# Optimization experiments

Hardware: AMD Instinct MI355X
Metric: run time of the kernel (lower is better)

The kernel has to match this reference:

```python
import jax, jax.numpy as jnp
import numpy as np

IN_FEATURES = 4096
OUT_FEATURES = 16384

def setup_inputs() -> dict:
    key = jax.random.key(0)
    k1, k2 = jax.random.split(key)
    x = jax.random.normal(k1, (4, 2048, IN_FEATURES), dtype=jnp.float32)
    # init_weights: uniform(-1, 1)
    W = jax.random.uniform(k2, (OUT_FEATURES, IN_FEATURES), dtype=jnp.float32, minval=-1.0, maxval=1.0)
    b = jnp.zeros((OUT_FEATURES,), dtype=jnp.float32)
    return {"x": x, "W": W, "b": b}

def reference(x, W, b):
    # Binarize weights to {-1, 0, +1} via sign, then dense linear: y = x @ sign(W)^T + b
    Wb = jnp.sign(W)
    return jnp.einsum('bsd,od->bso', x, Wb) + b
```

## Files before the change

### kernel.cpp

```cpp
#include <hip/hip_runtime.h>
#include <hip/hip_bf16.h>

#define M_TOT 8192
#define N_TOT 16384
#define K_TOT 4096
#define BM 256
#define BN 128
#define BK 64
#define NT (K_TOT / BK)

typedef int i32x4 __attribute__((ext_vector_type(4)));
typedef int i32x16 __attribute__((ext_vector_type(16)));
typedef __bf16 bf16x8 __attribute__((ext_vector_type(8)));
typedef float f32x4 __attribute__((ext_vector_type(4)));

#define GLOAD_LDS16(g, l)                                                     \
  __builtin_amdgcn_global_load_lds(                                           \
      (__attribute__((address_space(1))) const void*)(g),                     \
      (__attribute__((address_space(3))) void*)(l), 16, 0, 0)

__device__ __forceinline__ ushort f2bf_rne(float f) {
  unsigned u = __float_as_uint(f);
  u += 0x7FFFu + ((u >> 16) & 1u);
  return (ushort)(u >> 16);
}
__device__ __forceinline__ ushort sgn_bf16(float w) {
  return w > 0.f ? (ushort)0x3F80u : (w < 0.f ? (ushort)0xBF80u : (ushort)0u);
}


__global__ void quant_x_kernel(const float* __restrict__ x,
                               char* __restrict__ At, float* __restrict__ s) {
  int row = blockIdx.x;
  int tid = threadIdx.x;
  const float4* xr = (const float4*)(x + (size_t)row * K_TOT + tid * 16);
  float4 v[4];
  float amax = 0.f;
#pragma unroll
  for (int j = 0; j < 4; ++j) {
    v[j] = xr[j];
    amax = fmaxf(amax, fmaxf(fmaxf(fabsf(v[j].x), fabsf(v[j].y)),
                             fmaxf(fabsf(v[j].z), fabsf(v[j].w))));
  }
#pragma unroll
  for (int o = 32; o > 0; o >>= 1) amax = fmaxf(amax, __shfl_xor(amax, o));
  __shared__ float wmax[4];
  if ((tid & 63) == 0) wmax[tid >> 6] = amax;
  __syncthreads();
  amax = fmaxf(fmaxf(wmax[0], wmax[1]), fmaxf(wmax[2], wmax[3]));
  float inv = amax > 0.f ? 127.0f / amax : 0.f;
  if (tid == 0) s[row] = amax * (1.0f / 127.0f);
  int q[16];
#pragma unroll
  for (int j = 0; j < 4; ++j) {
    q[j * 4 + 0] = max(-127, min(127, __float2int_rn(v[j].x * inv)));
    q[j * 4 + 1] = max(-127, min(127, __float2int_rn(v[j].y * inv)));
    q[j * 4 + 2] = max(-127, min(127, __float2int_rn(v[j].z * inv)));
    q[j * 4 + 3] = max(-127, min(127, __float2int_rn(v[j].w * inv)));
  }
  int4 o4;
  int* op = (int*)&o4;
#pragma unroll
  for (int j = 0; j < 4; ++j)
    op[j] = (q[j * 4] & 255) | ((q[j * 4 + 1] & 255) << 8) |
            ((q[j * 4 + 2] & 255) << 16) | ((q[j * 4 + 3] & 255) << 24);
  int r32 = row >> 5, l31 = row & 31;
  int kt = tid >> 2, ks = (tid >> 1) & 1, hi = tid & 1;
  size_t dst = ((size_t)(r32 * 128 + kt * 2 + ks) << 10) + ((hi * 32 + l31) << 4);
  *(int4*)(At + dst) = o4;
}

__global__ void quant_w_kernel(const float* __restrict__ w,
                               char* __restrict__ Bt) {
  int n32 = blockIdx.x;
  int t = threadIdx.x;
#pragma unroll 4
  for (int i = 0; i < 32; ++i) {
    int c = i * 256 + t;
    int kt = c >> 7, ks = (c >> 6) & 1, l = c & 63;
    int n = n32 * 32 + (l & 31);
    int k = kt * 64 + ks * 32 + (l >> 5) * 16;
    const float4* src = (const float4*)(w + (size_t)n * K_TOT + k);
    int4 o4;
    int* op = (int*)&o4;
#pragma unroll
    for (int j = 0; j < 4; ++j) {
      float4 v = src[j];
      int q0 = v.x > 0.f ? 1 : (v.x < 0.f ? -1 : 0);
      int q1 = v.y > 0.f ? 1 : (v.y < 0.f ? -1 : 0);
      int q2 = v.z > 0.f ? 1 : (v.z < 0.f ? -1 : 0);
      int q3 = v.w > 0.f ? 1 : (v.w < 0.f ? -1 : 0);
      op[j] = (q0 & 255) | ((q1 & 255) << 8) | ((q2 & 255) << 16) |
              ((q3 & 255) << 24);
    }
    *(int4*)(Bt + ((size_t)n32 << 17) + ((size_t)c << 4)) = o4;
  }
}

__global__ __launch_bounds__(256, 2) void gemm_i8_reg(
    const char* __restrict__ At, const char* __restrict__ Bt,
    const float* __restrict__ s, const float* __restrict__ bias,
    float* __restrict__ C) {
  __shared__ char lds[4][16384];

  int bid = blockIdx.x;
  int wg = (bid & 7) * 512 + (bid >> 3);
  int bnS = wg >> 9;
  int rem = wg & 511;
  int bm = rem >> 4;
  int bn = bnS * 16 + (rem & 15);
  int rowBase = bm * BM;
  int colBase = bn * BN;

  int t = threadIdx.x;
  int lane = t & 63;
  int wave = t >> 6;
  int wr = wave >> 1;
  int wc = wave & 1;
  int l31 = lane & 31;
  int hi = lane >> 5;

  const char* gAp[4];
#pragma unroll
  for (int q = 0; q < 4; ++q) {
    int ss = t + 256 * q;
    int g = ss >> 6;
    int ks = g >> 3, rg = g & 7;
    gAp[q] = At + ((size_t)((bm * 8 + rg) * 128 + ks) << 10) + ((ss & 63) << 4);
  }
  const char* gBp[2];
#pragma unroll
  for (int ni = 0; ni < 2; ++ni)
    gBp[ni] = Bt + ((size_t)(bn * 4 + wc * 2 + ni) << 17) + (lane << 4);

  i32x16 acc[4][2] = {};
  i32x4 brA[2][2], brB[2][2];

#define STAGE_A(kt_, buf_)                                                    \
  {                                                                           \
    size_t _o = (size_t)(kt_) << 11;                                          \
    GLOAD_LDS16(gAp[0] + _o, &lds[buf_][t * 16]);                             \
    GLOAD_LDS16(gAp[1] + _o, &lds[buf_][4096 + t * 16]);                      \
    GLOAD_LDS16(gAp[2] + _o, &lds[buf_][8192 + t * 16]);                      \
    GLOAD_LDS16(gAp[3] + _o, &lds[buf_][12288 + t * 16]);                     \
  }
#define LOADB(kt_, dst)                                                       \
  {                                                                           \
    size_t _o = (size_t)(kt_) << 11;                                          \
    dst[0][0] = *(const i32x4*)(gBp[0] + _o);                                 \
    dst[0][1] = *(const i32x4*)(gBp[1] + _o);                                 \
    dst[1][0] = *(const i32x4*)(gBp[0] + _o + 1024);                          \
    dst[1][1] = *(const i32x4*)(gBp[1] + _o + 1024);                          \
  }
#define COMPUTE(buf_, bset)                                                   \
  {                                                                           \
    const char* _la = &lds[buf_][0];                                          \
    _Pragma("unroll") for (int ks = 0; ks < 2; ++ks) {                        \
      _Pragma("unroll") for (int mi = 0; mi < 4; ++mi) {                      \
        i32x4 _af = *(const i32x4*)(_la + ((ks * 8 + wr * 4 + mi) << 10) +    \
                                    (lane << 4));                             \
        acc[mi][0] = __builtin_amdgcn_mfma_i32_32x32x32_i8(                   \
            _af, bset[ks][0], acc[mi][0], 0, 0, 0);                           \
        acc[mi][1] = __builtin_amdgcn_mfma_i32_32x32x32_i8(                   \
            _af, bset[ks][1], acc[mi][1], 0, 0, 0);                           \
      }                                                                       \
    }                                                                         \
  }
#define TILE(kt_, buf_, bcur, bnxt, VMC)                                      \
  {                                                                           \
    STAGE_A((kt_) + 2, ((buf_) + 2) & 3);                                     \
    LOADB((kt_) + 1, bnxt);                                                   \
    asm volatile("s_waitcnt vmcnt(" #VMC ")" ::: "memory");                   \
    COMPUTE(buf_, bcur);                                                      \
    __builtin_amdgcn_s_barrier();                                             \
  }

  STAGE_A(0, 0);
  STAGE_A(1, 1);
  LOADB(0, brA);
  asm volatile("s_waitcnt vmcnt(0)" ::: "memory");
  __builtin_amdgcn_s_barrier();

  for (int it = 0; it < 15; ++it) {
    int kt = it * 4;
    TILE(kt + 0, 0, brA, brB, 8);
    TILE(kt + 1, 1, brB, brA, 8);
    TILE(kt + 2, 2, brA, brB, 8);
    TILE(kt + 3, 3, brB, brA, 8);
  }
  {
    STAGE_A(62, 2);
    LOADB(61, brB);
    asm volatile("s_waitcnt vmcnt(8)" ::: "memory");
    COMPUTE(0, brA);
    __builtin_amdgcn_s_barrier();

    STAGE_A(63, 3);
    LOADB(62, brA);
    asm volatile("s_waitcnt vmcnt(8)" ::: "memory");
    COMPUTE(1, brB);
    __builtin_amdgcn_s_barrier();

    LOADB(63, brB);
    asm volatile("s_waitcnt vmcnt(4)" ::: "memory");
    COMPUTE(2, brA);
    __builtin_amdgcn_s_barrier();

    asm volatile("s_waitcnt vmcnt(0)" ::: "memory");
    COMPUTE(3, brB);
  }

#undef TILE
#undef COMPUTE
#undef LOADB
#undef STAGE_A

#pragma unroll
  for (int mi = 0; mi < 4; ++mi) {
#pragma unroll
    for (int ni = 0; ni < 2; ++ni) {
      int gc = colBase + wc * 64 + ni * 32 + l31;
      float bv = bias[gc];
#pragma unroll
      for (int rg = 0; rg < 16; ++rg) {
        int rowIn = (rg & 3) + 8 * (rg >> 2) + 4 * hi;
        int gr = rowBase + wr * 128 + mi * 32 + rowIn;
        C[(size_t)gr * N_TOT + gc] = (float)acc[mi][ni][rg] * s[gr] + bv;
      }
    }
  }
}

__global__ void gemm_fused_kernel(const float* __restrict__ A,
                                  const float* __restrict__ W,
                                  const float* __restrict__ bias,
                                  float* __restrict__ C) {
  __shared__ ushort lsA[128 * 32];
  __shared__ ushort lsB[128 * 32];

  int nwg = gridDim.x;
  int bid = blockIdx.x;
  int wg = (bid & 7) * (nwg >> 3) + (bid >> 3);
  const int NBN = N_TOT / 128;
  int bm = wg / NBN;
  int bn = wg % NBN;
  int rowBase = bm * 128;
  int colBase = bn * 128;

  int t = threadIdx.x;
  int lane = t & 63;
  int wave = t >> 6;
  int wm = (wave >> 1) * 64;
  int wn = (wave & 1) * 64;

  f32x4 acc[4][4] = {};

  int srow = t >> 3;
  int scol = (t & 7) * 4;
  int fr = lane & 15;
  int koff = (lane >> 4) * 8;

  for (int k0 = 0; k0 < K_TOT; k0 += 32) {
    float4 va[4], vb[4];
#pragma unroll
    for (int r = 0; r < 4; ++r) {
      va[r] = *(const float4*)&A[(size_t)(rowBase + r * 32 + srow) * K_TOT + k0 + scol];
      vb[r] = *(const float4*)&W[(size_t)(colBase + r * 32 + srow) * K_TOT + k0 + scol];
    }
    __syncthreads();
#pragma unroll
    for (int r = 0; r < 4; ++r) {
      int e = r * 1024 + t * 4;
      ushort4 oa, ob;
      oa.x = f2bf_rne(va[r].x); oa.y = f2bf_rne(va[r].y);
      oa.z = f2bf_rne(va[r].z); oa.w = f2bf_rne(va[r].w);
      ob.x = sgn_bf16(vb[r].x); ob.y = sgn_bf16(vb[r].y);
      ob.z = sgn_bf16(vb[r].z); ob.w = sgn_bf16(vb[r].w);
      *(ushort4*)&lsA[e] = oa;
      *(ushort4*)&lsB[e] = ob;
    }
    __syncthreads();

    bf16x8 af[4], bfr[4];
#pragma unroll
    for (int i = 0; i < 4; ++i)
      af[i] = *(const bf16x8*)&lsA[(wm + i * 16 + fr) * 32 + koff];
#pragma unroll
    for (int j = 0; j < 4; ++j)
      bfr[j] = *(const bf16x8*)&lsB[(wn + j * 16 + fr) * 32 + koff];

#pragma unroll
    for (int i = 0; i < 4; ++i)
#pragma unroll
      for (int j = 0; j < 4; ++j)
        acc[i][j] = __builtin_amdgcn_mfma_f32_16x16x32_bf16(af[i], bfr[j],
                                                            acc[i][j], 0, 0, 0);
  }

  int orow0 = rowBase + wm + ((lane >> 4) << 2);
  int ocol0 = colBase + wn + (lane & 15);
#pragma unroll
  for (int i = 0; i < 4; ++i) {
#pragma unroll
    for (int j = 0; j < 4; ++j) {
      int col = ocol0 + j * 16;
      float bv = bias[col];
#pragma unroll
      for (int rg = 0; rg < 4; ++rg) {
        int row = orow0 + i * 16 + rg;
        C[(size_t)row * N_TOT + col] = acc[i][j][rg] + bv;
      }
    }
  }
}

extern "C" void kernel_launch(void* const* d_in, const int* in_sizes, int n_in,
                              void* d_out, int out_size, void* d_ws,
                              size_t ws_size, hipStream_t stream) {
  const float* x = (const float*)d_in[0];
  const float* W = (const float*)d_in[1];
  const float* b = (const float*)d_in[2];
  float* out = (float*)d_out;

  const size_t xq_bytes = (size_t)M_TOT * K_TOT;
  const size_t wq_bytes = (size_t)N_TOT * K_TOT;
  const size_t need = xq_bytes + wq_bytes + M_TOT * 4;

  if (ws_size >= need) {
    char* At = (char*)d_ws;
    char* Bt = At + xq_bytes;
    float* s = (float*)(Bt + wq_bytes);
    quant_x_kernel<<<M_TOT, 256, 0, stream>>>(x, At, s);
    quant_w_kernel<<<N_TOT / 32, 256, 0, stream>>>(W, Bt);
    const int nblocks = (M_TOT / BM) * (N_TOT / BN);
    gemm_i8_reg<<<nblocks, 256, 0, stream>>>(At, Bt, s, b, out);
  } else {
    const int nblocks = (M_TOT / 128) * (N_TOT / 128);
    gemm_fused_kernel<<<nblocks, 256, 0, stream>>>(x, W, b, out);
  }
}
```

Measured before the change: 744.9 us.

## Replace LDS-staged int8 GEMM with register-only direct-load kernel

Result: slower. 864.7 us (+16.1%).

```diff
diff --git a/kernel.cpp b/kernel.cpp
--- a/kernel.cpp
+++ b/kernel.cpp
@@ -4,20 +4,12 @@
 #define M_TOT 8192
 #define N_TOT 16384
 #define K_TOT 4096
-#define BM 256
-#define BN 128
-#define BK 64
-#define NT (K_TOT / BK)
+#define NT (K_TOT / 64)
 
 typedef int i32x4 __attribute__((ext_vector_type(4)));
 typedef int i32x16 __attribute__((ext_vector_type(16)));
 typedef __bf16 bf16x8 __attribute__((ext_vector_type(8)));
 typedef float f32x4 __attribute__((ext_vector_type(4)));
-
-#define GLOAD_LDS16(g, l)                                                     \
-  __builtin_amdgcn_global_load_lds(                                           \
-      (__attribute__((address_space(1))) const void*)(g),                     \
-      (__attribute__((address_space(3))) void*)(l), 16, 0, 0)
 
 __device__ __forceinline__ ushort f2bf_rne(float f) {
   unsigned u = __float_as_uint(f);
@@ -97,134 +89,81 @@
   }
 }
 
-__global__ __launch_bounds__(256, 2) void gemm_i8_reg(
+__global__ __launch_bounds__(256, 2) void gemm_i8_pure(
     const char* __restrict__ At, const char* __restrict__ Bt,
     const float* __restrict__ s, const float* __restrict__ bias,
     float* __restrict__ C) {
-  __shared__ char lds[4][16384];
-
   int bid = blockIdx.x;
-  int wg = (bid & 7) * 512 + (bid >> 3);
-  int bnS = wg >> 9;
-  int rem = wg & 511;
-  int bm = rem >> 4;
-  int bn = bnS * 16 + (rem & 15);
-  int rowBase = bm * BM;
-  int colBase = bn * BN;
-
-  int t = threadIdx.x;
-  int lane = t & 63;
-  int wave = t >> 6;
-  int wr = wave >> 1;
-  int wc = wave & 1;
+  int xcd = bid & 7;
+  int loc = bid >> 3;
+  int bm = (xcd >> 2) * 32 + (loc & 31);
+  int bnq = (xcd & 3) * 16 + (loc >> 5);
+  int lane = threadIdx.x & 63;
+  int wave = threadIdx.x >> 6;
+  int bn_w = bnq * 4 + wave;
+  int rowBase = bm * 128;
+  int colBase = bn_w * 64;
   int l31 = lane & 31;
   int hi = lane >> 5;
 
-  const char* gAp[4];
-#pragma unroll
-  for (int q = 0; q < 4; ++q) {
-    int ss = t + 256 * q;
-    int g = ss >> 6;
-    int ks = g >> 3, rg = g & 7;
-    gAp[q] = At + ((size_t)((bm * 8 + rg) * 128 + ks) << 10) + ((ss & 63) << 4);
-  }
-  const char* gBp[2];
-#pragma unroll
-  for (int ni = 0; ni < 2; ++ni)
-    gBp[ni] = Bt + ((size_t)(bn * 4 + wc * 2 + ni) << 17) + (lane << 4);
+  const char* pA0 = At + (((size_t)(bm * 4 + 0) * 128) << 10) + (lane << 4);
+  const char* pA1 = pA0 + (128 << 10);
+  const char* pA2 = pA0 + (256 << 10);
+  const char* pA3 = pA0 + (384 << 10);
+  const char* pB0 = Bt + (((size_t)(bn_w * 2 + 0) * 128) << 10) + (lane << 4);
+  const char* pB1 = pB0 + (128 << 10);
 
   i32x16 acc[4][2] = {};
-  i32x4 brA[2][2], brB[2][2];
-
-#define STAGE_A(kt_, buf_)                                                    \
+  i32x4 aP[4][2], bP[2][2], aQ[4][2], bQ[2][2];
+
+#define LOADSET(AS, BS, O)                                                    \
   {                                                                           \
-    size_t _o = (size_t)(kt_) << 11;                                          \
-    GLOAD_LDS16(gAp[0] + _o, &lds[buf_][t * 16]);                             \
-    GLOAD_LDS16(gAp[1] + _o, &lds[buf_][4096 + t * 16]);                      \
-    GLOAD_LDS16(gAp[2] + _o, &lds[buf_][8192 + t * 16]);                      \
-    GLOAD_LDS16(gAp[3] + _o, &lds[buf_][12288 + t * 16]);                     \
-  }
-#define LOADB(kt_, dst)                                                       \
-  {                                                                           \
-    size_t _o = (size_t)(kt_) << 11;                                          \
-    dst[0][0] = *(const i32x4*)(gBp[0] + _o);                                 \
-    dst[0][1] = *(const i32x4*)(gBp[1] + _o);                                 \
-    dst[1][0] = *(const i32x4*)(gBp[0] + _o + 1024);                          \
-    dst[1][1] = *(const i32x4*)(gBp[1] + _o + 1024);                          \
-  }
-#define COMPUTE(buf_, bset)                                                   \
-  {                                                                           \
-    const char* _la = &lds[buf_][0];                                          \
-    _Pragma("unroll") for (int ks = 0; ks < 2; ++ks) {                        \
-      _Pragma("unroll") for (int mi = 0; mi < 4; ++mi) {                      \
-        i32x4 _af = *(const i32x4*)(_la + ((ks * 8 + wr * 4 + mi) << 10) +    \
-                                    (lane << 4));                             \
-        acc[mi][0] = __builtin_amdgcn_mfma_i32_32x32x32_i8(                   \
-            _af, bset[ks][0], acc[mi][0], 0, 0, 0);                           \
-        acc[mi][1] = __builtin_amdgcn_mfma_i32_32x32x32_i8(                   \
-            _af, bset[ks][1], acc[mi][1], 0, 0, 0);                           \
-      }                                                                       \
-    }                                                                         \
-  }
-#define TILE(kt_, buf_, bcur, bnxt, VMC)                                      \
-  {                                                                           \
-    STAGE_A((kt_) + 2, ((buf_) + 2) & 3);                                     \
-    LOADB((kt_) + 1, bnxt);                                                   \
-    asm volatile("s_waitcnt vmcnt(" #VMC ")" ::: "memory");                   \
-    COMPUTE(buf_, bcur);                                                      \
-    __builtin_amdgcn_s_barrier();                                             \
-  }
-
-  STAGE_A(0, 0);
-  STAGE_A(1, 1);
-  LOADB(0, brA);
-  asm volatile("s_waitcnt vmcnt(0)" ::: "memory");
-  __builtin_amdgcn_s_barrier();
-
-  for (int it = 0; it < 15; ++it) {
-    int kt = it * 4;
-    TILE(kt + 0, 0, brA, brB, 8);
-    TILE(kt + 1, 1, brB, brA, 8);
-    TILE(kt + 2, 2, brA, brB, 8);
-    TILE(kt + 3, 3, brB, brA, 8);
-  }
-  {
-    STAGE_A(62, 2);
-    LOADB(61, brB);
-    asm volatile("s_waitcnt vmcnt(8)" ::: "memory");
-    COMPUTE(0, brA);
-    __builtin_amdgcn_s_barrier();
-
-    STAGE_A(63, 3);
-    LOADB(62, brA);
-    asm volatile("s_waitcnt vmcnt(8)" ::: "memory");
-    COMPUTE(1, brB);
-    __builtin_amdgcn_s_barrier();
-
-    LOADB(63, brB);
-    asm volatile("s_waitcnt vmcnt(4)" ::: "memory");
-    COMPUTE(2, brA);
-    __builtin_amdgcn_s_barrier();
-
-    asm volatile("s_waitcnt vmcnt(0)" ::: "memory");
-    COMPUTE(3, brB);
-  }
-
-#undef TILE
-#undef COMPUTE
-#undef LOADB
-#undef STAGE_A
+    AS[0][0] = *(const i32x4*)(pA0 + (O));                                    \
+    AS[0][1] = *(const i32x4*)(pA0 + (O) + 1024);                             \
+    AS[1][0] = *(const i32x4*)(pA1 + (O));                                    \
+    AS[1][1] = *(const i32x4*)(pA1 + (O) + 1024);                             \
+    AS[2][0] = *(const i32x4*)(pA2 + (O));                                    \
+    AS[2][1] = *(const i32x4*)(pA2 + (O) + 1024);                             \
+    AS[3][0] = *(const i32x4*)(pA3 + (O));                                    \
+    AS[3][1] = *(const i32x4*)(pA3 + (O) + 1024);                             \
+    BS[0][0] = *(const i32x4*)(pB0 + (O));                                    \
+    BS[0][1] = *(const i32x4*)(pB0 + (O) + 1024);                             \
+    BS[1][0] = *(const i32x4*)(pB1 + (O));                                    \
+    BS[1][1] = *(const i32x4*)(pB1 + (O) + 1024);                             \
+  }
+#define MFMASET(AS, BS)                                                       \
+  _Pragma("unroll") for (int ks = 0; ks < 2; ++ks)                            \
+      _Pragma("unroll") for (int mi = 0; mi < 4; ++mi)                        \
+          _Pragma("unroll") for (int ni = 0; ni < 2; ++ni)                    \
+              acc[mi][ni] = __builtin_amdgcn_mfma_i32_32x32x32_i8(            \
+                  AS[mi][ks], BS[ni][ks], acc[mi][ni], 0, 0, 0);
+
+  LOADSET(aP, bP, 0);
+  for (int it = 0; it < 31; ++it) {
+    LOADSET(aQ, bQ, 2048);
+    MFMASET(aP, bP);
+    pA0 += 4096; pA1 += 4096; pA2 += 4096; pA3 += 4096;
+    pB0 += 4096; pB1 += 4096;
+    LOADSET(aP, bP, 0);
+    MFMASET(aQ, bQ);
+  }
+  LOADSET(aQ, bQ, 2048);
+  MFMASET(aP, bP);
+  MFMASET(aQ, bQ);
+
+#undef MFMASET
+#undef LOADSET
 
 #pragma unroll
   for (int mi = 0; mi < 4; ++mi) {
 #pragma unroll
     for (int ni = 0; ni < 2; ++ni) {
-      int gc = colBase + wc * 64 + ni * 32 + l31;
+      int gc = colBase + ni * 32 + l31;
       float bv = bias[gc];
 #pragma unroll
       for (int rg = 0; rg < 16; ++rg) {
         int rowIn = (rg & 3) + 8 * (rg >> 2) + 4 * hi;
-        int gr = rowBase + wr * 128 + mi * 32 + rowIn;
+        int gr = rowBase + mi * 32 + rowIn;
         C[(size_t)gr * N_TOT + gc] = (float)acc[mi][ni][rg] * s[gr] + bv;
       }
     }
@@ -332,8 +271,7 @@
     float* s = (float*)(Bt + wq_bytes);
     quant_x_kernel<<<M_TOT, 256, 0, stream>>>(x, At, s);
     quant_w_kernel<<<N_TOT / 32, 256, 0, stream>>>(W, Bt);
-    const int nblocks = (M_TOT / BM) * (N_TOT / BN);
-    gemm_i8_reg<<<nblocks, 256, 0, stream>>>(At, Bt, s, b, out);
+    gemm_i8_pure<<<4096, 256, 0, stream>>>(At, Bt, s, b, out);
   } else {
     const int nblocks = (M_TOT / 128) * (N_TOT / 128);
     gemm_fused_kernel<<<nblocks, 256, 0, stream>>>(x, W, b, out);
```
